# Optimization experiments

Hardware: AMD Instinct MI355X
Metric: run time of the kernel (lower is better)

Reference implementation:

```python
import jax, jax.numpy as jnp
import numpy as np

N_NODES = 50000
N_EDGES = 800000
D_IN = 64
D_HID = 64
D_OUT = 64


def setup_inputs() -> dict:
    key = jax.random.key(0)
    ks = jax.random.split(key, 10)
    x = jax.random.normal(ks[0], (N_NODES, D_IN), dtype=jnp.float32)
    src = jax.random.randint(ks[1], (N_EDGES,), 0, N_NODES, dtype=jnp.int32)
    dst = jax.random.randint(ks[2], (N_EDGES,), 0, N_NODES, dtype=jnp.int32)
    s = 1.0 / np.sqrt(D_IN)
    W0 = jax.random.uniform(ks[3], (D_IN, D_HID), jnp.float32, -s, s)
    b0 = jnp.zeros((D_HID,), jnp.float32)
    W1 = jax.random.uniform(ks[4], (D_HID, D_HID), jnp.float32, -s, s)
    b1 = jnp.zeros((D_HID,), jnp.float32)
    W2 = jax.random.uniform(ks[5], (D_HID, D_OUT), jnp.float32, -s, s)
    b2 = jnp.zeros((D_OUT,), jnp.float32)
    return {"x": x, "src": src, "dst": dst, "W0": W0, "b0": b0,
            "W1": W1, "b1": b1, "W2": W2, "b2": b2}


def reference(x, src, dst, W0, b0, W1, b1, W2, b2):
    N = x.shape[0]
    # in-degree (constant across layers)
    deg = jax.ops.segment_sum(jnp.ones(src.shape[0], x.dtype), dst, num_segments=N)
    inv = (1.0 / (deg + 1.0))[:, None]  # [N,1] gcn normalizer (deg + self)

    def sage_gcn(h, W, b):
        # gather neighbor feats along edges, scatter-add to destinations
        agg = jax.ops.segment_sum(h[src], dst, num_segments=N)  # [N,d]
        h_neigh = (agg + h) * inv
        return h_neigh @ W + b

    h = sage_gcn(x, W0, b0)
    h = jax.nn.relu(h)
    h = sage_gcn(h, W1, b1)
    h = jax.nn.relu(h)
    h = sage_gcn(h, W2, b2)
    return h
```

## Files before the change

### kernel.cpp

```cpp
#include <hip/hip_runtime.h>
#include <hip/hip_fp16.h>

#define D 64
#define CAP 64

typedef _Float16 h2_t __attribute__((ext_vector_type(2)));

union u4 { float4 f4; __half2 h2[4]; };

union v16u {
    float4 f4;
    h2_t   h2[4];
};

__global__ __launch_bounds__(256) void init_cursor_kernel(int* __restrict__ cursor, int N) {
    int i = blockIdx.x * 256 + threadIdx.x;
    if (i < N) cursor[i] = i << 6;
}

__global__ __launch_bounds__(256) void fill_bucket_sliced_kernel(
    const int* __restrict__ src, const int* __restrict__ dst,
    int* __restrict__ cursor, int* __restrict__ col,
    int nE, int slice_size)
{
    const int g  = blockIdx.x & 7;
    const int gb = blockIdx.x >> 3;
    const int lo = g * slice_size;
    const int hi = lo + slice_size;
    int e4 = (gb * 256 + (int)threadIdx.x) * 4;
    if (e4 + 3 < nE) {
        int4 d = *(const int4*)(dst + e4);
        bool m0 = (d.x >= lo) & (d.x < hi);
        bool m1 = (d.y >= lo) & (d.y < hi);
        bool m2 = (d.z >= lo) & (d.z < hi);
        bool m3 = (d.w >= lo) & (d.w < hi);
        if (m0 | m1 | m2 | m3) {
            int4 s = *(const int4*)(src + e4);
            if (m0) { int k = atomicAdd(&cursor[d.x], 1); if (k < ((d.x + 1) << 6)) col[k] = s.x; }
            if (m1) { int k = atomicAdd(&cursor[d.y], 1); if (k < ((d.y + 1) << 6)) col[k] = s.y; }
            if (m2) { int k = atomicAdd(&cursor[d.z], 1); if (k < ((d.z + 1) << 6)) col[k] = s.z; }
            if (m3) { int k = atomicAdd(&cursor[d.w], 1); if (k < ((d.w + 1) << 6)) col[k] = s.w; }
        }
    } else if (e4 < nE) {
        for (int e = e4; e < nE; ++e) {
            int dd = dst[e];
            if (dd >= lo && dd < hi) {
                int k = atomicAdd(&cursor[dd], 1);
                if (k < ((dd + 1) << 6)) col[k] = src[e];
            }
        }
    }
}

template<bool IN32>
__global__ __launch_bounds__(256) void gemm_kernel(
    const void* __restrict__ hin, const float* __restrict__ W,
    __half* __restrict__ g, int N)
{
    const int j   = threadIdx.x & 63;
    const int wid = (blockIdx.x * blockDim.x + threadIdx.x) >> 6;
    const int nw  = (gridDim.x * blockDim.x) >> 6;

    h2_t wp[32];
    #pragma unroll
    for (int kk = 0; kk < 32; ++kk) {
        h2_t p;
        p[0] = (_Float16)W[(2 * kk + 0) * D + j];
        p[1] = (_Float16)W[(2 * kk + 1) * D + j];
        wp[kk] = p;
    }

    if constexpr (IN32) {
        const float4* __restrict__ x4 = (const float4*)hin;
        for (int r = wid; r < N; r += nw) {
            float4 buf[16];
            #pragma unroll
            for (int t = 0; t < 16; ++t) buf[t] = x4[(size_t)r * 16 + t];
            float o0 = 0.0f, o1 = 0.0f;
            #pragma unroll
            for (int t = 0; t < 16; ++t) {
                h2_t p0, p1;
                p0[0] = (_Float16)buf[t].x; p0[1] = (_Float16)buf[t].y;
                p1[0] = (_Float16)buf[t].z; p1[1] = (_Float16)buf[t].w;
                o0 = __builtin_amdgcn_fdot2(p0, wp[2 * t + 0], o0, false);
                o1 = __builtin_amdgcn_fdot2(p1, wp[2 * t + 1], o1, false);
            }
            g[(size_t)r * D + j] = __float2half(o0 + o1);
        }
    } else {
        const float4* __restrict__ hin4 = (const float4*)hin;
        for (int r = wid; r < N; r += nw) {
            v16u buf[8];
            #pragma unroll
            for (int t = 0; t < 8; ++t) buf[t].f4 = hin4[(size_t)r * 8 + t];
            float o0 = 0.0f, o1 = 0.0f;
            #pragma unroll
            for (int t = 0; t < 8; ++t) {
                o0 = __builtin_amdgcn_fdot2(buf[t].h2[0], wp[t * 4 + 0], o0, false);
                o1 = __builtin_amdgcn_fdot2(buf[t].h2[1], wp[t * 4 + 1], o1, false);
                o0 = __builtin_amdgcn_fdot2(buf[t].h2[2], wp[t * 4 + 2], o0, false);
                o1 = __builtin_amdgcn_fdot2(buf[t].h2[3], wp[t * 4 + 3], o1, false);
            }
            g[(size_t)r * D + j] = __float2half(o0 + o1);
        }
    }
}

template<bool OUT_H>
__global__ __launch_bounds__(256, 4) void agg_kernel(
    const __half* __restrict__ g, const int* __restrict__ cursor,
    const int* __restrict__ col, const float* __restrict__ bias,
    void* __restrict__ hout, int N, int do_relu)
{
    const int lane = threadIdx.x & 63;
    const int og   = lane >> 3;
    const int fo   = lane & 7;
    const int w    = threadIdx.x >> 6;

    const float4 bb0 = ((const float4*)bias)[fo * 2 + 0];
    const float4 bb1 = ((const float4*)bias)[fo * 2 + 1];

    const float4* __restrict__ g4 = (const float4*)g;

    const int nwaves = gridDim.x * 4;
    for (int i0 = blockIdx.x * 4 + w; i0 < N; i0 += nwaves) {
        const int i  = __builtin_amdgcn_readfirstlane(i0);
        const int rs = i << 6;
        int ce = cursor[i];
        ce = (ce < rs + CAP) ? ce : (rs + CAP);
        const int deg = ce - rs;

        int ee = rs + lane;
        int idxv = (ee < ce) ? col[ee] : 0;

        float4 aA0 = {0,0,0,0}, aA1 = {0,0,0,0};
        float4 aB0 = {0,0,0,0}, aB1 = {0,0,0,0};

        for (int e0 = 0; e0 < deg; e0 += 16) {
            int sA = __shfl(idxv, e0 + og);
            int sB = __shfl(idxv, e0 + 8 + og);
            u4 rA, rB;
            rA.f4 = g4[(size_t)sA * 8 + fo];
            rB.f4 = g4[(size_t)sB * 8 + fo];
            float mA = (e0 + og < deg) ? 1.0f : 0.0f;
            float mB = (e0 + 8 + og < deg) ? 1.0f : 0.0f;
            float2 p;
            p = __half22float2(rA.h2[0]); aA0.x = fmaf(mA, p.x, aA0.x); aA0.y = fmaf(mA, p.y, aA0.y);
            p = __half22float2(rA.h2[1]); aA0.z = fmaf(mA, p.x, aA0.z); aA0.w = fmaf(mA, p.y, aA0.w);
            p = __half22float2(rA.h2[2]); aA1.x = fmaf(mA, p.x, aA1.x); aA1.y = fmaf(mA, p.y, aA1.y);
            p = __half22float2(rA.h2[3]); aA1.z = fmaf(mA, p.x, aA1.z); aA1.w = fmaf(mA, p.y, aA1.w);
            p = __half22float2(rB.h2[0]); aB0.x = fmaf(mB, p.x, aB0.x); aB0.y = fmaf(mB, p.y, aB0.y);
            p = __half22float2(rB.h2[1]); aB0.z = fmaf(mB, p.x, aB0.z); aB0.w = fmaf(mB, p.y, aB0.w);
            p = __half22float2(rB.h2[2]); aB1.x = fmaf(mB, p.x, aB1.x); aB1.y = fmaf(mB, p.y, aB1.y);
            p = __half22float2(rB.h2[3]); aB1.z = fmaf(mB, p.x, aB1.z); aB1.w = fmaf(mB, p.y, aB1.w);
        }

        float4 t0, t1;
        t0.x = aA0.x + aB0.x; t0.y = aA0.y + aB0.y;
        t0.z = aA0.z + aB0.z; t0.w = aA0.w + aB0.w;
        t1.x = aA1.x + aB1.x; t1.y = aA1.y + aB1.y;
        t1.z = aA1.z + aB1.z; t1.w = aA1.w + aB1.w;
        t0.x += __shfl_xor(t0.x, 8); t0.x += __shfl_xor(t0.x, 16); t0.x += __shfl_xor(t0.x, 32);
        t0.y += __shfl_xor(t0.y, 8); t0.y += __shfl_xor(t0.y, 16); t0.y += __shfl_xor(t0.y, 32);
        t0.z += __shfl_xor(t0.z, 8); t0.z += __shfl_xor(t0.z, 16); t0.z += __shfl_xor(t0.z, 32);
        t0.w += __shfl_xor(t0.w, 8); t0.w += __shfl_xor(t0.w, 16); t0.w += __shfl_xor(t0.w, 32);
        t1.x += __shfl_xor(t1.x, 8); t1.x += __shfl_xor(t1.x, 16); t1.x += __shfl_xor(t1.x, 32);
        t1.y += __shfl_xor(t1.y, 8); t1.y += __shfl_xor(t1.y, 16); t1.y += __shfl_xor(t1.y, 32);
        t1.z += __shfl_xor(t1.z, 8); t1.z += __shfl_xor(t1.z, 16); t1.z += __shfl_xor(t1.z, 32);
        t1.w += __shfl_xor(t1.w, 8); t1.w += __shfl_xor(t1.w, 16); t1.w += __shfl_xor(t1.w, 32);

        u4 sv; sv.f4 = g4[(size_t)i * 8 + fo];
        float2 s0 = __half22float2(sv.h2[0]);
        float2 s1 = __half22float2(sv.h2[1]);
        float2 s2 = __half22float2(sv.h2[2]);
        float2 s3 = __half22float2(sv.h2[3]);
        float invd = 1.0f / (float)(deg + 1);
        float4 o0, o1;
        o0.x = fmaf(t0.x + s0.x, invd, bb0.x);
        o0.y = fmaf(t0.y + s0.y, invd, bb0.y);
        o0.z = fmaf(t0.z + s1.x, invd, bb0.z);
        o0.w = fmaf(t0.w + s1.y, invd, bb0.w);
        o1.x = fmaf(t1.x + s2.x, invd, bb1.x);
        o1.y = fmaf(t1.y + s2.y, invd, bb1.y);
        o1.z = fmaf(t1.z + s3.x, invd, bb1.z);
        o1.w = fmaf(t1.w + s3.y, invd, bb1.w);
        if (do_relu) {
            o0.x = fmaxf(o0.x, 0.0f); o0.y = fmaxf(o0.y, 0.0f);
            o0.z = fmaxf(o0.z, 0.0f); o0.w = fmaxf(o0.w, 0.0f);
            o1.x = fmaxf(o1.x, 0.0f); o1.y = fmaxf(o1.y, 0.0f);
            o1.z = fmaxf(o1.z, 0.0f); o1.w = fmaxf(o1.w, 0.0f);
        }
        if (og == 0) {
            if constexpr (OUT_H) {
                u4 o;
                o.h2[0] = __floats2half2_rn(o0.x, o0.y);
                o.h2[1] = __floats2half2_rn(o0.z, o0.w);
                o.h2[2] = __floats2half2_rn(o1.x, o1.y);
                o.h2[3] = __floats2half2_rn(o1.z, o1.w);
                ((float4*)hout)[(size_t)i * 8 + fo] = o.f4;
            } else {
                ((float4*)hout)[(size_t)i * 16 + fo * 2 + 0] = o0;
                ((float4*)hout)[(size_t)i * 16 + fo * 2 + 1] = o1;
            }
        }
    }
}

extern "C" void kernel_launch(void* const* d_in, const int* in_sizes, int n_in,
                              void* d_out, int out_size, void* d_ws, size_t ws_size,
                              hipStream_t stream) {
    const float* x   = (const float*)d_in[0];
    const int*   src = (const int*)d_in[1];
    const int*   dst = (const int*)d_in[2];
    const float* W0  = (const float*)d_in[3];
    const float* b0  = (const float*)d_in[4];
    const float* W1  = (const float*)d_in[5];
    const float* b1  = (const float*)d_in[6];
    const float* W2  = (const float*)d_in[7];
    const float* b2  = (const float*)d_in[8];
    float* out = (float*)d_out;

    const int N = in_sizes[0] / D;
    const int E = in_sizes[1];

    char* ws = (char*)d_ws;
    size_t off = 0;
    auto alloc = [&](size_t bytes) -> void* {
        void* p = ws + off;
        off = (off + bytes + 255) & ~(size_t)255;
        return p;
    };
    int*    cursor = (int*)   alloc((size_t)N * sizeof(int));
    int*    col    = (int*)   alloc((size_t)N * CAP * sizeof(int));
    __half* gbuf   = (__half*)alloc((size_t)N * D * sizeof(__half));
    __half* h1     = (__half*)alloc((size_t)N * D * sizeof(__half));
    __half* h2     = (__half*)alloc((size_t)N * D * sizeof(__half));

    const int n_blocks = (N + 255) / 256;
    init_cursor_kernel<<<n_blocks, 256, 0, stream>>>(cursor, N);
    const int e4_blocks = (E / 4 + 255) / 256;
    const int slice_size = (N + 7) / 8;
    fill_bucket_sliced_kernel<<<e4_blocks * 8, 256, 0, stream>>>(src, dst, cursor, col, E, slice_size);

    const int gemm_blocks = 1024;
    const int agg_blocks  = 4096;

    gemm_kernel<true ><<<gemm_blocks, 256, 0, stream>>>(x,  W0, gbuf, N);
    agg_kernel<true ><<<agg_blocks, 256, 0, stream>>>(gbuf, cursor, col, b0, h1,  N, 1);
    gemm_kernel<false><<<gemm_blocks, 256, 0, stream>>>(h1, W1, gbuf, N);
    agg_kernel<true ><<<agg_blocks, 256, 0, stream>>>(gbuf, cursor, col, b1, h2,  N, 1);
    gemm_kernel<false><<<gemm_blocks, 256, 0, stream>>>(h2, W2, gbuf, N);
    agg_kernel<false><<<agg_blocks, 256, 0, stream>>>(gbuf, cursor, col, b2, out, N, 0);
}
```

Measured before the change: 248.6 us.

## Split features into two 32-column planes and aggregate each half separately

Stores the intermediate features as two planar half-width buffers and runs the neighbor aggregation twice, once per 32-column half. Each pass gathers from a table half the size, aiming to improve cache hit rate for the random gathers. The cost is reading the adjacency list twice, extra kernel launches, and smaller per-lane loads. The column-index load is also made nontemporal.

```diff
diff --git a/kernel.cpp b/kernel.cpp
--- a/kernel.cpp
+++ b/kernel.cpp
@@ -6,7 +6,7 @@
 
 typedef _Float16 h2_t __attribute__((ext_vector_type(2)));
 
-union u4 { float4 f4; __half2 h2[4]; };
+union u2v { float2 f2; __half2 h2[2]; };
 
 union v16u {
     float4 f4;
@@ -54,8 +54,9 @@
 
 template<bool IN32>
 __global__ __launch_bounds__(256) void gemm_kernel(
-    const void* __restrict__ hin, const float* __restrict__ W,
-    __half* __restrict__ g, int N)
+    const void* __restrict__ hin_lo, const void* __restrict__ hin_hi,
+    const float* __restrict__ W,
+    __half* __restrict__ g_lo, __half* __restrict__ g_hi, int N)
 {
     const int j   = threadIdx.x & 63;
     const int wid = (blockIdx.x * blockDim.x + threadIdx.x) >> 6;
@@ -70,8 +71,11 @@
         wp[kk] = p;
     }
 
+    __half* __restrict__ gout = (j < 32) ? g_lo : g_hi;
+    const int jc = j & 31;
+
     if constexpr (IN32) {
-        const float4* __restrict__ x4 = (const float4*)hin;
+        const float4* __restrict__ x4 = (const float4*)hin_lo;
         for (int r = wid; r < N; r += nw) {
             float4 buf[16];
             #pragma unroll
@@ -85,14 +89,17 @@
                 o0 = __builtin_amdgcn_fdot2(p0, wp[2 * t + 0], o0, false);
                 o1 = __builtin_amdgcn_fdot2(p1, wp[2 * t + 1], o1, false);
             }
-            g[(size_t)r * D + j] = __float2half(o0 + o1);
+            gout[(size_t)r * 32 + jc] = __float2half(o0 + o1);
         }
     } else {
-        const float4* __restrict__ hin4 = (const float4*)hin;
+        const float4* __restrict__ lo4 = (const float4*)hin_lo;
+        const float4* __restrict__ hi4 = (const float4*)hin_hi;
         for (int r = wid; r < N; r += nw) {
             v16u buf[8];
             #pragma unroll
-            for (int t = 0; t < 8; ++t) buf[t].f4 = hin4[(size_t)r * 8 + t];
+            for (int t = 0; t < 4; ++t) buf[t].f4     = lo4[(size_t)r * 4 + t];
+            #pragma unroll
+            for (int t = 0; t < 4; ++t) buf[4 + t].f4 = hi4[(size_t)r * 4 + t];
             float o0 = 0.0f, o1 = 0.0f;
             #pragma unroll
             for (int t = 0; t < 8; ++t) {
@@ -101,26 +108,26 @@
                 o0 = __builtin_amdgcn_fdot2(buf[t].h2[2], wp[t * 4 + 2], o0, false);
                 o1 = __builtin_amdgcn_fdot2(buf[t].h2[3], wp[t * 4 + 3], o1, false);
             }
-            g[(size_t)r * D + j] = __float2half(o0 + o1);
+            gout[(size_t)r * 32 + jc] = __float2half(o0 + o1);
         }
     }
 }
 
 template<bool OUT_H>
-__global__ __launch_bounds__(256, 4) void agg_kernel(
-    const __half* __restrict__ g, const int* __restrict__ cursor,
-    const int* __restrict__ col, const float* __restrict__ bias,
-    void* __restrict__ hout, int N, int do_relu)
+__global__ __launch_bounds__(256, 4) void agg_half_kernel(
+    const __half* __restrict__ gH,
+    const int* __restrict__ cursor, const int* __restrict__ col,
+    const float* __restrict__ bias,
+    void* __restrict__ houtH,
+    int H, int N, int do_relu)
 {
     const int lane = threadIdx.x & 63;
     const int og   = lane >> 3;
     const int fo   = lane & 7;
     const int w    = threadIdx.x >> 6;
 
-    const float4 bb0 = ((const float4*)bias)[fo * 2 + 0];
-    const float4 bb1 = ((const float4*)bias)[fo * 2 + 1];
-
-    const float4* __restrict__ g4 = (const float4*)g;
+    const float4 bb = ((const float4*)bias)[H * 8 + fo];
+    const float2* __restrict__ g2 = (const float2*)gH;
 
     const int nwaves = gridDim.x * 4;
     for (int i0 = blockIdx.x * 4 + w; i0 < N; i0 += nwaves) {
@@ -131,76 +138,54 @@
         const int deg = ce - rs;
 
         int ee = rs + lane;
-        int idxv = (ee < ce) ? col[ee] : 0;
-
-        float4 aA0 = {0,0,0,0}, aA1 = {0,0,0,0};
-        float4 aB0 = {0,0,0,0}, aB1 = {0,0,0,0};
+        int idxv = (ee < ce) ? __builtin_nontemporal_load(&col[ee]) : 0;
+
+        float4 aA = {0,0,0,0}, aB = {0,0,0,0};
 
         for (int e0 = 0; e0 < deg; e0 += 16) {
             int sA = __shfl(idxv, e0 + og);
             int sB = __shfl(idxv, e0 + 8 + og);
-            u4 rA, rB;
-            rA.f4 = g4[(size_t)sA * 8 + fo];
-            rB.f4 = g4[(size_t)sB * 8 + fo];
+            u2v vA, vB;
+            vA.f2 = g2[(size_t)sA * 8 + fo];
+            vB.f2 = g2[(size_t)sB * 8 + fo];
             float mA = (e0 + og < deg) ? 1.0f : 0.0f;
             float mB = (e0 + 8 + og < deg) ? 1.0f : 0.0f;
             float2 p;
-            p = __half22float2(rA.h2[0]); aA0.x = fmaf(mA, p.x, aA0.x); aA0.y = fmaf(mA, p.y, aA0.y);
-            p = __half22float2(rA.h2[1]); aA0.z = fmaf(mA, p.x, aA0.z); aA0.w = fmaf(mA, p.y, aA0.w);
-            p = __half22float2(rA.h2[2]); aA1.x = fmaf(mA, p.x, aA1.x); aA1.y = fmaf(mA, p.y, aA1.y);
-            p = __half22float2(rA.h2[3]); aA1.z = fmaf(mA, p.x, aA1.z); aA1.w = fmaf(mA, p.y, aA1.w);
-            p = __half22float2(rB.h2[0]); aB0.x = fmaf(mB, p.x, aB0.x); aB0.y = fmaf(mB, p.y, aB0.y);
-            p = __half22float2(rB.h2[1]); aB0.z = fmaf(mB, p.x, aB0.z); aB0.w = fmaf(mB, p.y, aB0.w);
-            p = __half22float2(rB.h2[2]); aB1.x = fmaf(mB, p.x, aB1.x); aB1.y = fmaf(mB, p.y, aB1.y);
-            p = __half22float2(rB.h2[3]); aB1.z = fmaf(mB, p.x, aB1.z); aB1.w = fmaf(mB, p.y, aB1.w);
-        }
-
-        float4 t0, t1;
-        t0.x = aA0.x + aB0.x; t0.y = aA0.y + aB0.y;
-        t0.z = aA0.z + aB0.z; t0.w = aA0.w + aB0.w;
-        t1.x = aA1.x + aB1.x; t1.y = aA1.y + aB1.y;
-        t1.z = aA1.z + aB1.z; t1.w = aA1.w + aB1.w;
-        t0.x += __shfl_xor(t0.x, 8); t0.x += __shfl_xor(t0.x, 16); t0.x += __shfl_xor(t0.x, 32);
-        t0.y += __shfl_xor(t0.y, 8); t0.y += __shfl_xor(t0.y, 16); t0.y += __shfl_xor(t0.y, 32);
-        t0.z += __shfl_xor(t0.z, 8); t0.z += __shfl_xor(t0.z, 16); t0.z += __shfl_xor(t0.z, 32);
-        t0.w += __shfl_xor(t0.w, 8); t0.w += __shfl_xor(t0.w, 16); t0.w += __shfl_xor(t0.w, 32);
-        t1.x += __shfl_xor(t1.x, 8); t1.x += __shfl_xor(t1.x, 16); t1.x += __shfl_xor(t1.x, 32);
-        t1.y += __shfl_xor(t1.y, 8); t1.y += __shfl_xor(t1.y, 16); t1.y += __shfl_xor(t1.y, 32);
-        t1.z += __shfl_xor(t1.z, 8); t1.z += __shfl_xor(t1.z, 16); t1.z += __shfl_xor(t1.z, 32);
-        t1.w += __shfl_xor(t1.w, 8); t1.w += __shfl_xor(t1.w, 16); t1.w += __shfl_xor(t1.w, 32);
-
-        u4 sv; sv.f4 = g4[(size_t)i * 8 + fo];
+            p = __half22float2(vA.h2[0]); aA.x = fmaf(mA, p.x, aA.x); aA.y = fmaf(mA, p.y, aA.y);
+            p = __half22float2(vA.h2[1]); aA.z = fmaf(mA, p.x, aA.z); aA.w = fmaf(mA, p.y, aA.w);
+            p = __half22float2(vB.h2[0]); aB.x = fmaf(mB, p.x, aB.x); aB.y = fmaf(mB, p.y, aB.y);
+            p = __half22float2(vB.h2[1]); aB.z = fmaf(mB, p.x, aB.z); aB.w = fmaf(mB, p.y, aB.w);
+        }
+
+        float4 t;
+        t.x = aA.x + aB.x; t.y = aA.y + aB.y;
+        t.z = aA.z + aB.z; t.w = aA.w + aB.w;
+        t.x += __shfl_xor(t.x, 8); t.x += __shfl_xor(t.x, 16); t.x += __shfl_xor(t.x, 32);
+        t.y += __shfl_xor(t.y, 8); t.y += __shfl_xor(t.y, 16); t.y += __shfl_xor(t.y, 32);
+        t.z += __shfl_xor(t.z, 8); t.z += __shfl_xor(t.z, 16); t.z += __shfl_xor(t.z, 32);
+        t.w += __shfl_xor(t.w, 8); t.w += __shfl_xor(t.w, 16); t.w += __shfl_xor(t.w, 32);
+
+        u2v sv; sv.f2 = g2[(size_t)i * 8 + fo];
         float2 s0 = __half22float2(sv.h2[0]);
         float2 s1 = __half22float2(sv.h2[1]);
-        float2 s2 = __half22float2(sv.h2[2]);
-        float2 s3 = __half22float2(sv.h2[3]);
         float invd = 1.0f / (float)(deg + 1);
-        float4 o0, o1;
-        o0.x = fmaf(t0.x + s0.x, invd, bb0.x);
-        o0.y = fmaf(t0.y + s0.y, invd, bb0.y);
-        o0.z = fmaf(t0.z + s1.x, invd, bb0.z);
-        o0.w = fmaf(t0.w + s1.y, invd, bb0.w);
-        o1.x = fmaf(t1.x + s2.x, invd, bb1.x);
-        o1.y = fmaf(t1.y + s2.y, invd, bb1.y);
-        o1.z = fmaf(t1.z + s3.x, invd, bb1.z);
-        o1.w = fmaf(t1.w + s3.y, invd, bb1.w);
+        float4 o;
+        o.x = fmaf(t.x + s0.x, invd, bb.x);
+        o.y = fmaf(t.y + s0.y, invd, bb.y);
+        o.z = fmaf(t.z + s1.x, invd, bb.z);
+        o.w = fmaf(t.w + s1.y, invd, bb.w);
         if (do_relu) {
-            o0.x = fmaxf(o0.x, 0.0f); o0.y = fmaxf(o0.y, 0.0f);
-            o0.z = fmaxf(o0.z, 0.0f); o0.w = fmaxf(o0.w, 0.0f);
-            o1.x = fmaxf(o1.x, 0.0f); o1.y = fmaxf(o1.y, 0.0f);
-            o1.z = fmaxf(o1.z, 0.0f); o1.w = fmaxf(o1.w, 0.0f);
+            o.x = fmaxf(o.x, 0.0f); o.y = fmaxf(o.y, 0.0f);
+            o.z = fmaxf(o.z, 0.0f); o.w = fmaxf(o.w, 0.0f);
         }
         if (og == 0) {
             if constexpr (OUT_H) {
-                u4 o;
-                o.h2[0] = __floats2half2_rn(o0.x, o0.y);
-                o.h2[1] = __floats2half2_rn(o0.z, o0.w);
-                o.h2[2] = __floats2half2_rn(o1.x, o1.y);
-                o.h2[3] = __floats2half2_rn(o1.z, o1.w);
-                ((float4*)hout)[(size_t)i * 8 + fo] = o.f4;
+                u2v ov;
+                ov.h2[0] = __floats2half2_rn(o.x, o.y);
+                ov.h2[1] = __floats2half2_rn(o.z, o.w);
+                ((float2*)houtH)[(size_t)i * 8 + fo] = ov.f2;
             } else {
-                ((float4*)hout)[(size_t)i * 16 + fo * 2 + 0] = o0;
-                ((float4*)hout)[(size_t)i * 16 + fo * 2 + 1] = o1;
+                ((float4*)houtH)[(size_t)i * 16 + H * 8 + fo] = o;
             }
         }
     }
@@ -230,11 +215,15 @@
         off = (off + bytes + 255) & ~(size_t)255;
         return p;
     };
+    const size_t half_bytes = (size_t)N * 32 * sizeof(__half);
     int*    cursor = (int*)   alloc((size_t)N * sizeof(int));
     int*    col    = (int*)   alloc((size_t)N * CAP * sizeof(int));
-    __half* gbuf   = (__half*)alloc((size_t)N * D * sizeof(__half));
-    __half* h1     = (__half*)alloc((size_t)N * D * sizeof(__half));
-    __half* h2     = (__half*)alloc((size_t)N * D * sizeof(__half));
+    __half* g_lo   = (__half*)alloc(half_bytes);
+    __half* g_hi   = (__half*)alloc(half_bytes);
+    __half* h1_lo  = (__half*)alloc(half_bytes);
+    __half* h1_hi  = (__half*)alloc(half_bytes);
+    __half* h2_lo  = (__half*)alloc(half_bytes);
+    __half* h2_hi  = (__half*)alloc(half_bytes);
 
     const int n_blocks = (N + 255) / 256;
     init_cursor_kernel<<<n_blocks, 256, 0, stream>>>(cursor, N);
@@ -245,10 +234,13 @@
     const int gemm_blocks = 1024;
     const int agg_blocks  = 4096;
 
-    gemm_kernel<true ><<<gemm_blocks, 256, 0, stream>>>(x,  W0, gbuf, N);
-    agg_kernel<true ><<<agg_blocks, 256, 0, stream>>>(gbuf, cursor, col, b0, h1,  N, 1);
-    gemm_kernel<false><<<gemm_blocks, 256, 0, stream>>>(h1, W1, gbuf, N);
-    agg_kernel<true ><<<agg_blocks, 256, 0, stream>>>(gbuf, cursor, col, b1, h2,  N, 1);
-    gemm_kernel<false><<<gemm_blocks, 256, 0, stream>>>(h2, W2, gbuf, N);
-    agg_kernel<false><<<agg_blocks, 256, 0, stream>>>(gbuf, cursor, col, b2, out, N, 0);
-}
+    gemm_kernel<true ><<<gemm_blocks, 256, 0, stream>>>(x, nullptr, W0, g_lo, g_hi, N);
+    agg_half_kernel<true ><<<agg_blocks, 256, 0, stream>>>(g_lo, cursor, col, b0, h1_lo, 0, N, 1);
+    agg_half_kernel<true ><<<agg_blocks, 256, 0, stream>>>(g_hi, cursor, col, b0, h1_hi, 1, N, 1);
+    gemm_kernel<false><<<gemm_blocks, 256, 0, stream>>>(h1_lo, h1_hi, W1, g_lo, g_hi, N);
+    agg_half_kernel<true ><<<agg_blocks, 256, 0, stream>>>(g_lo, cursor, col, b1, h2_lo, 0, N, 1);
+    agg_half_kernel<true ><<<agg_blocks, 256, 0, stream>>>(g_hi, cursor, col, b1, h2_hi, 1, N, 1);
+    gemm_kernel<false><<<gemm_blocks, 256, 0, stream>>>(h2_lo, h2_hi, W2, g_lo, g_hi, N);
+    agg_half_kernel<false><<<agg_blocks, 256, 0, stream>>>(g_lo, cursor, col, b2, out, 0, N, 0);
+    agg_half_kernel<false><<<agg_blocks, 256, 0, stream>>>(g_hi, cursor, col, b2, out, 1, N, 0);
+}
```

Result: slower. 281.4 us (+13.2%).
